# Optimization experiments

Measured on AMD Instinct MI355X. Metric: run time of the kernel, lower is better.

The kernel has to match this reference:

```python
import jax, jax.numpy as jnp
import numpy as np
import math

D_MODEL = 512
N_HEAD = 8
D_FF = 2048
B, S, S_ENC = 2, 2048, 2048
EPS = 1e-5


def _linear_params(key, d_in, d_out):
    kw, kb = jax.random.split(key)
    w = jax.random.normal(kw, (d_in, d_out), dtype=jnp.float32) * 0.02
    b = jax.random.normal(kb, (d_out,), dtype=jnp.float32) * 0.02
    return w, b


def setup_inputs() -> dict:
    key = jax.random.key(0)
    ks = jax.random.split(key, 16)
    dec = jax.random.normal(ks[0], (B, S, D_MODEL), dtype=jnp.float32)
    enc = jax.random.normal(ks[1], (B, S_ENC, D_MODEL), dtype=jnp.float32)
    src_mask = jnp.ones((B, 1, 1, S_ENC), dtype=jnp.int32)  # no padding
    tgt_mask = jnp.tril(jnp.ones((S, S), dtype=jnp.int32))[None, None]  # causal
    inp = {"dec": dec, "enc": enc, "src_mask": src_mask, "tgt_mask": tgt_mask}
    # self-attention projections
    for i, nm in enumerate(["sa_wq", "sa_wk", "sa_wv", "sa_wo"]):
        w, b = _linear_params(ks[2 + i], D_MODEL, D_MODEL)
        inp[nm], inp[nm.replace("w", "b")] = w, b
    # cross-attention projections
    for i, nm in enumerate(["ca_wq", "ca_wk", "ca_wv", "ca_wo"]):
        w, b = _linear_params(ks[6 + i], D_MODEL, D_MODEL)
        inp[nm], inp[nm.replace("w", "b")] = w, b
    # FFN
    inp["ffn_w1"], inp["ffn_b1"] = _linear_params(ks[10], D_MODEL, D_FF)
    inp["ffn_w2"], inp["ffn_b2"] = _linear_params(ks[11], D_FF, D_MODEL)
    # LayerNorms (gamma=1, beta=0 init as in torch)
    for i in (1, 2, 3):
        inp[f"ln{i}_g"] = jnp.ones((D_MODEL,), dtype=jnp.float32)
        inp[f"ln{i}_b"] = jnp.zeros((D_MODEL,), dtype=jnp.float32)
    return inp


def _layer_norm(x, g, b):
    mu = jnp.mean(x, axis=-1, keepdims=True)
    var = jnp.mean(jnp.square(x - mu), axis=-1, keepdims=True)
    return (x - mu) * jax.lax.rsqrt(var + EPS) * g + b


def _mha(xq, xkv, wq, bq, wk, bk, wv, bv, wo, bo, mask):
    Bq, Sq, D = xq.shape
    Sk = xkv.shape[1]
    d_k = D // N_HEAD
    def split(x, s):
        return x.reshape(x.shape[0], s, N_HEAD, d_k).transpose(0, 2, 1, 3)  # [B,H,S,dk]
    q = split(xq @ wq + bq, Sq)
    k = split(xkv @ wk + bk, Sk)
    v = split(xkv @ wv + bv, Sk)
    scores = jnp.einsum("bhqd,bhkd->bhqk", q, k) / math.sqrt(d_k)
    if mask is not None:
        scores = jnp.where(mask == 0, jnp.float32(-1e9), scores)
    attn = jax.nn.softmax(scores, axis=-1)
    out = jnp.einsum("bhqk,bhkd->bhqd", attn, v)
    out = out.transpose(0, 2, 1, 3).reshape(Bq, Sq, D)
    return out @ wo + bo


def reference(dec, enc, src_mask, tgt_mask,
              sa_wq, sa_bq, sa_wk, sa_bk, sa_wv, sa_bv, sa_wo, sa_bo,
              ca_wq, ca_bq, ca_wk, ca_bk, ca_wv, ca_bv, ca_wo, ca_bo,
              ffn_w1, ffn_b1, ffn_w2, ffn_b2,
              ln1_g, ln1_b, ln2_g, ln2_b, ln3_g, ln3_b):
    # dropout is identity in eval mode
    x = _mha(dec, dec, sa_wq, sa_bq, sa_wk, sa_bk, sa_wv, sa_bv, sa_wo, sa_bo, tgt_mask)
    x = _layer_norm(x + dec, ln1_g, ln1_b)
    _x = x
    x = _mha(x, enc, ca_wq, ca_bq, ca_wk, ca_bk, ca_wv, ca_bv, ca_wo, ca_bo, src_mask)
    x = _layer_norm(x + _x, ln2_g, ln2_b)
    _x = x
    x = jax.nn.relu(x @ ffn_w1 + ffn_b1) @ ffn_w2 + ffn_b2
    x = _layer_norm(x + _x, ln3_g, ln3_b)
    return x
```

## Files before the change

kernel.cpp:

```cpp
#include <hip/hip_runtime.h>


#define D_MODEL 512
#define NHEAD 8
#define DK 64
#define SEQ 2048
#define MTOK 4096
#define DFF 2048

typedef __attribute__((ext_vector_type(8))) short bf16x8;
typedef __attribute__((ext_vector_type(4))) float f32x4;

#if __has_builtin(__builtin_amdgcn_exp2f)
#define EXP2(x) __builtin_amdgcn_exp2f(x)
#else
#define EXP2(x) exp2f(x)
#endif

__device__ __forceinline__ unsigned short f2bf(float x) {
  unsigned u = __float_as_uint(x);
  u += 0x7FFF + ((u >> 16) & 1);
  return (unsigned short)(u >> 16);
}
__device__ __forceinline__ unsigned pack2(float a, float b) {
  return (unsigned)f2bf(a) | ((unsigned)f2bf(b) << 16);
}
__device__ __forceinline__ unsigned cvtpk(float lo, float hi) {
  unsigned r;
  asm("v_cvt_pk_bf16_f32 %0, %1, %2" : "=v"(r) : "v"(lo), "v"(hi));
  return r;
}
__device__ __forceinline__ void load_lds16(const unsigned short* g, unsigned short* l) {
  __builtin_amdgcn_global_load_lds(
      (const __attribute__((address_space(1))) void*)g,
      (__attribute__((address_space(3))) void*)l, 16, 0, 0);
}

struct WDesc { const float* src; unsigned short* dst; int K; int N; };
struct WPack { WDesc d[10]; };

__global__ __launch_bounds__(256)
void wprep_kernel(WPack p) {
  const WDesc wd = p.d[blockIdx.y];
  const int ntx = wd.N >> 5;
  const int ntile = (wd.K >> 5) * ntx;
  if ((int)blockIdx.x >= ntile) return;
  const int n0 = (blockIdx.x % ntx) * 32;
  const int k0 = (blockIdx.x / ntx) * 32;
  __shared__ float T[32][33];
  const int tid = threadIdx.x;
  {
    const int r = tid >> 3, c4 = (tid & 7) * 4;
    float4 v = *(const float4*)(wd.src + (long)(k0 + r) * wd.N + n0 + c4);
    T[r][c4] = v.x; T[r][c4 + 1] = v.y; T[r][c4 + 2] = v.z; T[r][c4 + 3] = v.w;
  }
  __syncthreads();
  {
    const int n = tid >> 3, kq = (tid & 7) * 4;
    ushort4 o;
    o.x = f2bf(T[kq + 0][n]); o.y = f2bf(T[kq + 1][n]);
    o.z = f2bf(T[kq + 2][n]); o.w = f2bf(T[kq + 3][n]);
    *(ushort4*)(wd.dst + (long)(n0 + n) * wd.K + k0 + kq) = o;
  }
}

__global__ __launch_bounds__(256)
void cast_kernel(const float* __restrict__ s, unsigned short* __restrict__ d, int n8) {
  const int i = blockIdx.x * 256 + threadIdx.x;
  if (i >= n8) return;
  float4 a = *(const float4*)(s + (long)i * 8);
  float4 b = *(const float4*)(s + (long)i * 8 + 4);
  uint4 o;
  o.x = pack2(a.x, a.y); o.y = pack2(a.z, a.w);
  o.z = pack2(b.x, b.y); o.w = pack2(b.z, b.w);
  *(uint4*)(d + (long)i * 8) = o;
}

template<int MODE, int BM, int BN>
__global__ __launch_bounds__(256)
void gemm_bf16(const unsigned short* __restrict__ A, const unsigned short* __restrict__ Wt,
               const float* __restrict__ b0, const float* __restrict__ b1,
               const float* __restrict__ b2, const float* res,
               const float* __restrict__ lnm, const float* __restrict__ lnr,
               const float* __restrict__ lng, const float* __restrict__ lnbt,
               unsigned short* __restrict__ o0, unsigned short* __restrict__ o1,
               unsigned short* __restrict__ o2, float* of,
               int M, int N, int K, float scale0) {
  constexpr int MF = BM / 32, NF = BN / 32;
  constexpr int AI = BM / 64, BI = BN / 64;
  __shared__ unsigned short As[BM * 32];
  __shared__ unsigned short Bs[BN * 32];
  const int tid = threadIdx.x;
  const int w = tid >> 6, lane = tid & 63, g = lane >> 4, li = lane & 15;
  const int m0 = blockIdx.x * BM, n0 = blockIdx.y * BN;
  const int wm = w >> 1, wn = w & 1;

  f32x4 acc[MF][NF] = {};
  const unsigned short* Ap[AI];
  const unsigned short* Bp[BI];
#pragma unroll
  for (int i = 0; i < AI; i++) {
    const int idx = i * 256 + tid;
    Ap[i] = A + (long)(m0 + (idx % BM)) * K + (idx / BM) * 8;
  }
#pragma unroll
  for (int i = 0; i < BI; i++) {
    const int idx = i * 256 + tid;
    Bp[i] = Wt + (long)(n0 + (idx % BN)) * K + (idx / BN) * 8;
  }

  for (int k0 = 0; k0 < K; k0 += 32) {
    __syncthreads();
#pragma unroll
    for (int i = 0; i < AI; i++) load_lds16(Ap[i] + k0, &As[(i * 256 + w * 64) * 8]);
#pragma unroll
    for (int i = 0; i < BI; i++) load_lds16(Bp[i] + k0, &Bs[(i * 256 + w * 64) * 8]);
    __syncthreads();
    bf16x8 af[MF], bfr[NF];
#pragma unroll
    for (int mf = 0; mf < MF; mf++)
      af[mf] = *(const bf16x8*)&As[(g * BM + wm * (BM / 2) + mf * 16 + li) * 8];
#pragma unroll
    for (int nf = 0; nf < NF; nf++)
      bfr[nf] = *(const bf16x8*)&Bs[(g * BN + wn * (BN / 2) + nf * 16 + li) * 8];
#pragma unroll
    for (int mf = 0; mf < MF; mf++)
#pragma unroll
      for (int nf = 0; nf < NF; nf++)
        acc[mf][nf] = __builtin_amdgcn_mfma_f32_16x16x32_bf16(af[mf], bfr[nf], acc[mf][nf], 0, 0, 0);
  }

#pragma unroll
  for (int nf = 0; nf < NF; nf++) {
    const int c = n0 + wn * (BN / 2) + nf * 16 + li;
    float bias, scl = 1.f;
    unsigned short* hdst = nullptr;
    float lngv = 0.f, lnbv = 0.f;
    if constexpr (MODE == 0) {
      const int which = c >> 9;
      bias = (which == 0 ? b0 : (which == 1 ? b1 : b2))[c & 511];
      if (which == 0) scl = scale0;
      hdst = which == 0 ? o0 : (which == 1 ? o1 : o2);
    } else {
      bias = b0[c];
      if constexpr (MODE == 3) { lngv = lng[c]; lnbv = lnbt[c]; }
    }
#pragma unroll
    for (int mf = 0; mf < MF; mf++) {
#pragma unroll
      for (int j = 0; j < 4; j++) {
        const int r = m0 + wm * (BM / 2) + mf * 16 + g * 4 + j;
        float v = acc[mf][nf][j] + bias;
        if constexpr (MODE == 0) {
          v *= scl;
          const int b = r >> 11, s = r & (SEQ - 1), h = (c >> 6) & 7, d = c & 63;
          hdst[(((long)(b * NHEAD + h)) * SEQ + s) * DK + d] = f2bf(v);
        } else if constexpr (MODE == 1) {
          v += res[(long)r * N + c];
          of[(long)r * N + c] = v;
        } else if constexpr (MODE == 2) {
          o0[(long)r * N + c] = f2bf(fmaxf(v, 0.f));
        } else {
          const float xr = res[(long)r * N + c];
          v += (xr - lnm[r]) * lnr[r] * lngv + lnbv;
          of[(long)r * N + c] = v;
        }
      }
    }
  }
}

template<bool CAUSAL>
__global__ __launch_bounds__(256)
void attn_bf16(const unsigned short* __restrict__ Qg, const unsigned short* __restrict__ Kg,
               const unsigned short* __restrict__ Vg, float* __restrict__ Opart,
               float* __restrict__ Mst, float* __restrict__ Lst) {
  __shared__ unsigned short SM[16384];
  unsigned short* const Qp = SM;
  unsigned short* const Kp = SM + 8192;
  unsigned short* const Vt = SM + 12288;
  const int tid = threadIdx.x;
  const int w = tid >> 6, lane = tid & 63, g = lane >> 4, li = lane & 15;
  const int qb = blockIdx.x, bh = blockIdx.y, ck = blockIdx.z;
  const int q0 = qb * 128;
  const long base = (long)bh * SEQ * DK;
  unsigned short* const Pl = SM + w * 2048;

#pragma unroll
  for (int i = 0; i < 4; i++) {
    const int idx = i * 256 + tid;
    const int dg = idx >> 7, q = idx & 127;
    load_lds16(Qg + base + (long)(q0 + q) * DK + dg * 8, &Qp[(i * 256 + w * 64) * 8]);
  }
  __syncthreads();
  bf16x8 bq[2][2];
#pragma unroll
  for (int qf = 0; qf < 2; qf++)
#pragma unroll
    for (int ks = 0; ks < 2; ks++)
      bq[qf][ks] = *(const bf16x8*)&Qp[((ks * 4 + g) * 128 + w * 32 + qf * 16 + li) * 8];

  f32x4 oacc[2][4] = {};
  float mrun[2] = {-1e30f, -1e30f};
  float denom[2] = {0.f, 0.f};

  const int vdg = tid >> 5;
  const int vs0 = (tid & 31) * 2;
  const int vsg = vs0 >> 3, vso = vs0 & 7;

  const int tbeg = CAUSAL ? ck : ck * 8;
  const int tend = CAUSAL ? (2 * qb + 2) : (ck * 8 + 8);
  const int tstep = CAUSAL ? 4 : 1;
  for (int t = tbeg; t < tend; t += tstep) {
    const int k0 = t * 64;
    __syncthreads();
#pragma unroll
    for (int i = 0; i < 2; i++) {
      const int idx = i * 256 + tid;
      const int dg = idx >> 6, kk = idx & 63;
      load_lds16(Kg + base + (long)(k0 + kk) * DK + dg * 8, &Kp[(i * 256 + w * 64) * 8]);
    }
    {
      const unsigned short* vsrc = Vg + base + (long)(k0 + vs0) * DK + vdg * 8;
      uint4 r0 = *(const uint4*)vsrc;
      uint4 r1 = *(const uint4*)(vsrc + DK);
      unsigned short u0[8], u1[8];
      *(uint4*)u0 = r0; *(uint4*)u1 = r1;
#pragma unroll
      for (int e = 0; e < 8; e++) {
        const int d = vdg * 8 + e;
        const int dsw = d ^ (vsg & 7);
        *(unsigned*)&Vt[(vsg * 64 + dsw) * 8 + vso] =
            (unsigned)u0[e] | ((unsigned)u1[e] << 16);
      }
    }
    __syncthreads();

    f32x4 sacc[4][2] = {};
#pragma unroll
    for (int ks = 0; ks < 2; ks++) {
#pragma unroll
      for (int kf = 0; kf < 4; kf++) {
        bf16x8 ka = *(const bf16x8*)&Kp[((ks * 4 + g) * 64 + kf * 16 + li) * 8];
#pragma unroll
        for (int qf = 0; qf < 2; qf++)
          sacc[kf][qf] = __builtin_amdgcn_mfma_f32_16x16x32_bf16(ka, bq[qf][ks], sacc[kf][qf], 0, 0, 0);
      }
    }
    if (CAUSAL && t >= 2 * qb) {
#pragma unroll
      for (int kf = 0; kf < 4; kf++)
#pragma unroll
        for (int qf = 0; qf < 2; qf++)
#pragma unroll
          for (int j = 0; j < 4; j++) {
            const int kg_ = k0 + kf * 16 + g * 4 + j;
            const int qg_ = q0 + w * 32 + qf * 16 + li;
            if (kg_ > qg_) sacc[kf][qf][j] = -1e30f;
          }
    }
    float mx[2];
#pragma unroll
    for (int qf = 0; qf < 2; qf++) {
      float a = fmaxf(fmaxf(sacc[0][qf][0], sacc[0][qf][1]), fmaxf(sacc[0][qf][2], sacc[0][qf][3]));
      float b = fmaxf(fmaxf(sacc[1][qf][0], sacc[1][qf][1]), fmaxf(sacc[1][qf][2], sacc[1][qf][3]));
      float c = fmaxf(fmaxf(sacc[2][qf][0], sacc[2][qf][1]), fmaxf(sacc[2][qf][2], sacc[2][qf][3]));
      float d = fmaxf(fmaxf(sacc[3][qf][0], sacc[3][qf][1]), fmaxf(sacc[3][qf][2], sacc[3][qf][3]));
      float m_ = fmaxf(fmaxf(a, b), fmaxf(c, d));
      m_ = fmaxf(m_, __shfl_xor(m_, 16, 64));
      m_ = fmaxf(m_, __shfl_xor(m_, 32, 64));
      mx[qf] = m_;
    }
    const int full = !__all((mx[0] - mrun[0] <= 8.f) && (mx[1] - mrun[1] <= 8.f));
    float corrv[2] = {1.f, 1.f};
    if (full) {
#pragma unroll
      for (int qf = 0; qf < 2; qf++) {
        const float mn = fmaxf(mrun[qf], mx[qf]);
        corrv[qf] = EXP2(mrun[qf] - mn);
        mrun[qf] = mn;
      }
    }
#pragma unroll
    for (int qf = 0; qf < 2; qf++) {
      float ps = 0.f;
#pragma unroll
      for (int kf = 0; kf < 4; kf++)
#pragma unroll
        for (int j = 0; j < 4; j++) {
          const float p = EXP2(sacc[kf][qf][j] - mrun[qf]);
          sacc[kf][qf][j] = p;
          ps += p;
        }
      ps += __shfl_xor(ps, 16, 64);
      ps += __shfl_xor(ps, 32, 64);
      denom[qf] = denom[qf] * corrv[qf] + ps;
    }
    if (full) {
#pragma unroll
      for (int mf = 0; mf < 2; mf++)
#pragma unroll
        for (int j = 0; j < 4; j++) {
          const float cf = __shfl(corrv[mf], g * 4 + j, 64);
#pragma unroll
          for (int df = 0; df < 4; df++) oacc[mf][df][j] *= cf;
        }
    }
#pragma unroll
    for (int kf = 0; kf < 4; kf++)
#pragma unroll
      for (int qf = 0; qf < 2; qf++) {
        uint2 pv;
        pv.x = cvtpk(sacc[kf][qf][0], sacc[kf][qf][1]);
        pv.y = cvtpk(sacc[kf][qf][2], sacc[kf][qf][3]);
        *(uint2*)&Pl[((kf * 2 + (g >> 1)) * 32 + qf * 16 + li) * 8 + (g & 1) * 4] = pv;
      }
#pragma unroll
    for (int ks2 = 0; ks2 < 2; ks2++) {
      const int sg = ks2 * 4 + g;
#pragma unroll
      for (int mf = 0; mf < 2; mf++) {
        bf16x8 pa = *(const bf16x8*)&Pl[(sg * 32 + mf * 16 + li) * 8];
#pragma unroll
        for (int df = 0; df < 4; df++) {
          bf16x8 vb = *(const bf16x8*)&Vt[(sg * 64 + ((df * 16 + li) ^ (sg & 7))) * 8];
          oacc[mf][df] = __builtin_amdgcn_mfma_f32_16x16x32_bf16(pa, vb, oacc[mf][df], 0, 0, 0);
        }
      }
    }
  }

  const long pbase = (long)(ck * 16 + bh) * SEQ;
  if (g == 0) {
#pragma unroll
    for (int qf = 0; qf < 2; qf++) {
      const int q = q0 + w * 32 + qf * 16 + li;
      Mst[pbase + q] = mrun[qf];
      Lst[pbase + q] = denom[qf];
    }
  }
#pragma unroll
  for (int mf = 0; mf < 2; mf++)
#pragma unroll
    for (int j = 0; j < 4; j++) {
      const int q = q0 + w * 32 + mf * 16 + g * 4 + j;
      float* op = Opart + (pbase + q) * 64;
#pragma unroll
      for (int df = 0; df < 4; df++) op[df * 16 + li] = oacc[mf][df][j];
    }
}

__global__ __launch_bounds__(256)
void combine_kernel(const float* __restrict__ Opart, const float* __restrict__ Mst,
                    const float* __restrict__ Lst, unsigned short* __restrict__ AOb) {
  const int row = blockIdx.x * 4 + (threadIdx.x >> 6);
  const int lane = threadIdx.x & 63;
  const int bh = row >> 11, q = row & (SEQ - 1);
  float m[4], l[4], mstar = -1e30f;
#pragma unroll
  for (int c = 0; c < 4; c++) {
    m[c] = Mst[((long)c * 16 + bh) * SEQ + q];
    l[c] = Lst[((long)c * 16 + bh) * SEQ + q];
    mstar = fmaxf(mstar, m[c]);
  }
  float den = 0.f, o = 0.f;
#pragma unroll
  for (int c = 0; c < 4; c++) {
    const float wgt = EXP2(m[c] - mstar);
    den += wgt * l[c];
    o += wgt * Opart[(((long)c * 16 + bh) * SEQ + q) * 64 + lane];
  }
  const int b = bh >> 3, h = bh & 7;
  AOb[((long)(b * SEQ + q)) * D_MODEL + h * DK + lane] = f2bf(o / den);
}

template<int V>
__global__ __launch_bounds__(256)
void ln_kernel(const float* __restrict__ x, const float* __restrict__ gam,
               const float* __restrict__ bet, float* __restrict__ outf,
               unsigned short* __restrict__ outb, float* __restrict__ mu_s,
               float* __restrict__ rs_s) {
  const int row = blockIdx.x * 4 + (threadIdx.x >> 6);
  const int lane = threadIdx.x & 63;
  const float* xr = x + (long)row * D_MODEL;
  float4 v0 = *(const float4*)&xr[lane * 8];
  float4 v1 = *(const float4*)&xr[lane * 8 + 4];
  float xv[8] = {v0.x, v0.y, v0.z, v0.w, v1.x, v1.y, v1.z, v1.w};
  float s = 0.f, s2 = 0.f;
#pragma unroll
  for (int i = 0; i < 8; i++) { s += xv[i]; s2 = fmaf(xv[i], xv[i], s2); }
#pragma unroll
  for (int off = 32; off > 0; off >>= 1) {
    s += __shfl_xor(s, off, 64);
    s2 += __shfl_xor(s2, off, 64);
  }
  const float mu = s * (1.f / D_MODEL);
  const float var = fmaxf(s2 * (1.f / D_MODEL) - mu * mu, 0.f);
  const float rstd = rsqrtf(var + 1e-5f);
  float y[8];
#pragma unroll
  for (int i = 0; i < 8; i++) {
    const int c = lane * 8 + i;
    y[i] = (xv[i] - mu) * rstd * gam[c] + bet[c];
  }
  if constexpr (V == 0) {
    uint4 o;
    o.x = pack2(y[0], y[1]); o.y = pack2(y[2], y[3]);
    o.z = pack2(y[4], y[5]); o.w = pack2(y[6], y[7]);
    *(uint4*)(outb + (long)row * D_MODEL + lane * 8) = o;
    if (lane == 0) { mu_s[row] = mu; rs_s[row] = rstd; }
  } else {
    float* orow = outf + (long)row * D_MODEL + lane * 8;
    *(float4*)orow = make_float4(y[0], y[1], y[2], y[3]);
    *(float4*)(orow + 4) = make_float4(y[4], y[5], y[6], y[7]);
  }
}

extern "C" void kernel_launch(void* const* d_in, const int* in_sizes, int n_in,
                              void* d_out, int out_size, void* d_ws, size_t ws_size,
                              hipStream_t stream) {
  const float* dec = (const float*)d_in[0];
  const float* enc = (const float*)d_in[1];
  const float* sa_wq = (const float*)d_in[4];
  const float* sa_bq = (const float*)d_in[5];
  const float* sa_wk = (const float*)d_in[6];
  const float* sa_bk = (const float*)d_in[7];
  const float* sa_wv = (const float*)d_in[8];
  const float* sa_bv = (const float*)d_in[9];
  const float* sa_wo = (const float*)d_in[10];
  const float* sa_bo = (const float*)d_in[11];
  const float* ca_wq = (const float*)d_in[12];
  const float* ca_bq = (const float*)d_in[13];
  const float* ca_wk = (const float*)d_in[14];
  const float* ca_bk = (const float*)d_in[15];
  const float* ca_wv = (const float*)d_in[16];
  const float* ca_bv = (const float*)d_in[17];
  const float* ca_wo = (const float*)d_in[18];
  const float* ca_bo = (const float*)d_in[19];
  const float* ffn_w1 = (const float*)d_in[20];
  const float* ffn_b1 = (const float*)d_in[21];
  const float* ffn_w2 = (const float*)d_in[22];
  const float* ffn_b2 = (const float*)d_in[23];
  const float* ln1_g = (const float*)d_in[24];
  const float* ln1_b = (const float*)d_in[25];
  const float* ln2_g = (const float*)d_in[26];
  const float* ln2_b = (const float*)d_in[27];
  const float* ln3_g = (const float*)d_in[28];
  const float* ln3_b = (const float*)d_in[29];

  char* wsb = (char*)d_ws;
  unsigned short* dec_bf = (unsigned short*)wsb;
  float* Opart = (float*)wsb;
  float* Mst = (float*)(wsb + 33554432);
  float* Lst = (float*)(wsb + 34078720);
  unsigned short* MIDb = (unsigned short*)wsb;
  size_t off = 34603008;
  unsigned short* qkv_t = (unsigned short*)(wsb + off); off += 1572864;
  unsigned short* wo_t  = (unsigned short*)(wsb + off); off += 524288;
  unsigned short* cq_t  = (unsigned short*)(wsb + off); off += 524288;
  unsigned short* ckv_t = (unsigned short*)(wsb + off); off += 1048576;
  unsigned short* co_t  = (unsigned short*)(wsb + off); off += 524288;
  unsigned short* f1_t  = (unsigned short*)(wsb + off); off += 2097152;
  unsigned short* f2_t  = (unsigned short*)(wsb + off); off += 2097152;
  unsigned short* enc_bf = (unsigned short*)(wsb + off); off += 4194304;
  unsigned short* Qb  = (unsigned short*)(wsb + off); off += 4194304;
  unsigned short* Kb  = (unsigned short*)(wsb + off); off += 4194304;
  unsigned short* Vb  = (unsigned short*)(wsb + off); off += 4194304;
  unsigned short* AOb = (unsigned short*)(wsb + off); off += 4194304;
  unsigned short* X1b = (unsigned short*)(wsb + off); off += 4194304;
  unsigned short* X2b = (unsigned short*)(wsb + off); off += 4194304;
  float* R   = (float*)(wsb + off); off += 8388608;
  float* mu1 = (float*)(wsb + off); off += 16384;
  float* rs1 = (float*)(wsb + off); off += 16384;
  float* mu2 = (float*)(wsb + off); off += 16384;
  float* rs2 = (float*)(wsb + off); off += 16384;

  dim3 blk(256);
  const float QS = 0.125f * 1.44269504f;

  WPack wp;
  wp.d[0] = {sa_wq, qkv_t, 512, 512};
  wp.d[1] = {sa_wk, qkv_t + 262144, 512, 512};
  wp.d[2] = {sa_wv, qkv_t + 524288, 512, 512};
  wp.d[3] = {sa_wo, wo_t, 512, 512};
  wp.d[4] = {ca_wq, cq_t, 512, 512};
  wp.d[5] = {ca_wk, ckv_t, 512, 512};
  wp.d[6] = {ca_wv, ckv_t + 262144, 512, 512};
  wp.d[7] = {ca_wo, co_t, 512, 512};
  wp.d[8] = {ffn_w1, f1_t, 512, 2048};
  wp.d[9] = {ffn_w2, f2_t, 2048, 512};
  wprep_kernel<<<dim3(1024, 10), blk, 0, stream>>>(wp);
  cast_kernel<<<1024, blk, 0, stream>>>(dec, dec_bf, 262144);
  cast_kernel<<<1024, blk, 0, stream>>>(enc, enc_bf, 262144);

  gemm_bf16<0, 128, 128><<<dim3(32, 12), blk, 0, stream>>>(dec_bf, qkv_t, sa_bq, sa_bk, sa_bv,
      nullptr, nullptr, nullptr, nullptr, nullptr, Qb, Kb, Vb, nullptr, MTOK, 1536, 512, QS);
  attn_bf16<true><<<dim3(16, 16, 4), blk, 0, stream>>>(Qb, Kb, Vb, Opart, Mst, Lst);
  combine_kernel<<<8192, blk, 0, stream>>>(Opart, Mst, Lst, AOb);
  gemm_bf16<1, 128, 64><<<dim3(32, 8), blk, 0, stream>>>(AOb, wo_t, sa_bo, nullptr, nullptr,
      dec, nullptr, nullptr, nullptr, nullptr, nullptr, nullptr, nullptr, R, MTOK, 512, 512, 1.f);
  ln_kernel<0><<<1024, blk, 0, stream>>>(R, ln1_g, ln1_b, nullptr, X1b, mu1, rs1);

  gemm_bf16<0, 128, 64><<<dim3(32, 8), blk, 0, stream>>>(X1b, cq_t, ca_bq, nullptr, nullptr,
      nullptr, nullptr, nullptr, nullptr, nullptr, Qb, nullptr, nullptr, nullptr, MTOK, 512, 512, QS);
  gemm_bf16<0, 128, 128><<<dim3(32, 8), blk, 0, stream>>>(enc_bf, ckv_t, ca_bk, ca_bv, nullptr,
      nullptr, nullptr, nullptr, nullptr, nullptr, Kb, Vb, nullptr, nullptr, MTOK, 1024, 512, 1.f);
  attn_bf16<false><<<dim3(16, 16, 4), blk, 0, stream>>>(Qb, Kb, Vb, Opart, Mst, Lst);
  combine_kernel<<<8192, blk, 0, stream>>>(Opart, Mst, Lst, AOb);
  gemm_bf16<3, 128, 64><<<dim3(32, 8), blk, 0, stream>>>(AOb, co_t, ca_bo, nullptr, nullptr,
      R, mu1, rs1, ln1_g, ln1_b, nullptr, nullptr, nullptr, R, MTOK, 512, 512, 1.f);
  ln_kernel<0><<<1024, blk, 0, stream>>>(R, ln2_g, ln2_b, nullptr, X2b, mu2, rs2);

  gemm_bf16<2, 128, 128><<<dim3(32, 16), blk, 0, stream>>>(X2b, f1_t, ffn_b1, nullptr, nullptr,
      nullptr, nullptr, nullptr, nullptr, nullptr, MIDb, nullptr, nullptr, nullptr, MTOK, 2048, 512, 1.f);
  gemm_bf16<3, 128, 64><<<dim3(32, 8), blk, 0, stream>>>(MIDb, f2_t, ffn_b2, nullptr, nullptr,
      R, mu2, rs2, ln2_g, ln2_b, nullptr, nullptr, nullptr, R, MTOK, 512, 2048, 1.f);
  ln_kernel<1><<<1024, blk, 0, stream>>>(R, ln3_g, ln3_b, (float*)d_out, nullptr, nullptr, nullptr);
}
```

Baseline: 435.5 us.

## Double-buffer LDS tiles with K-step 64 in bf16 GEMM

```diff
diff --git a/kernel.cpp b/kernel.cpp
--- a/kernel.cpp
+++ b/kernel.cpp
@@ -87,9 +87,12 @@
                unsigned short* __restrict__ o2, float* of,
                int M, int N, int K, float scale0) {
   constexpr int MF = BM / 32, NF = BN / 32;
-  constexpr int AI = BM / 64, BI = BN / 64;
-  __shared__ unsigned short As[BM * 32];
-  __shared__ unsigned short Bs[BN * 32];
+  constexpr int AI = BM / 32;
+  constexpr int BI = BN / 32;
+  __shared__ unsigned short As0[BM * 64];
+  __shared__ unsigned short As1[BM * 64];
+  __shared__ unsigned short Bs0[BN * 64];
+  __shared__ unsigned short Bs1[BN * 64];
   const int tid = threadIdx.x;
   const int w = tid >> 6, lane = tid & 63, g = lane >> 4, li = lane & 15;
   const int m0 = blockIdx.x * BM, n0 = blockIdx.y * BN;
@@ -108,27 +111,44 @@
     const int idx = i * 256 + tid;
     Bp[i] = Wt + (long)(n0 + (idx % BN)) * K + (idx / BN) * 8;
   }
-
-  for (int k0 = 0; k0 < K; k0 += 32) {
+  const int nt = K >> 6;
+
+#define G_STAGE(t, Ad, Bd)                                               \
+  {                                                                      \
+    _Pragma("unroll") for (int i = 0; i < AI; i++)                       \
+        load_lds16(Ap[i] + (t) * 64, &Ad[(i * 256 + w * 64) * 8]);       \
+    _Pragma("unroll") for (int i = 0; i < BI; i++)                       \
+        load_lds16(Bp[i] + (t) * 64, &Bd[(i * 256 + w * 64) * 8]);       \
+  }
+
+#define G_COMP(Ad, Bd)                                                            \
+  {                                                                               \
+    _Pragma("unroll") for (int s = 0; s < 2; s++) {                               \
+      bf16x8 af[MF], bfr[NF];                                                     \
+      _Pragma("unroll") for (int mf = 0; mf < MF; mf++)                           \
+          af[mf] = *(const bf16x8*)&Ad[((s * 4 + g) * BM + wm * (BM / 2) + mf * 16 + li) * 8]; \
+      _Pragma("unroll") for (int nf = 0; nf < NF; nf++)                           \
+          bfr[nf] = *(const bf16x8*)&Bd[((s * 4 + g) * BN + wn * (BN / 2) + nf * 16 + li) * 8]; \
+      _Pragma("unroll") for (int mf = 0; mf < MF; mf++)                           \
+          _Pragma("unroll") for (int nf = 0; nf < NF; nf++)                       \
+              acc[mf][nf] = __builtin_amdgcn_mfma_f32_16x16x32_bf16(af[mf], bfr[nf], acc[mf][nf], 0, 0, 0); \
+    }                                                                             \
+  }
+
+  G_STAGE(0, As0, Bs0);
+  __syncthreads();
+  for (int t = 0; t < nt; t += 2) {
+    if (t + 1 < nt) G_STAGE(t + 1, As1, Bs1);
+    G_COMP(As0, Bs0);
     __syncthreads();
-#pragma unroll
-    for (int i = 0; i < AI; i++) load_lds16(Ap[i] + k0, &As[(i * 256 + w * 64) * 8]);
-#pragma unroll
-    for (int i = 0; i < BI; i++) load_lds16(Bp[i] + k0, &Bs[(i * 256 + w * 64) * 8]);
-    __syncthreads();
-    bf16x8 af[MF], bfr[NF];
-#pragma unroll
-    for (int mf = 0; mf < MF; mf++)
-      af[mf] = *(const bf16x8*)&As[(g * BM + wm * (BM / 2) + mf * 16 + li) * 8];
-#pragma unroll
-    for (int nf = 0; nf < NF; nf++)
-      bfr[nf] = *(const bf16x8*)&Bs[(g * BN + wn * (BN / 2) + nf * 16 + li) * 8];
-#pragma unroll
-    for (int mf = 0; mf < MF; mf++)
-#pragma unroll
-      for (int nf = 0; nf < NF; nf++)
-        acc[mf][nf] = __builtin_amdgcn_mfma_f32_16x16x32_bf16(af[mf], bfr[nf], acc[mf][nf], 0, 0, 0);
-  }
+    if (t + 1 < nt) {
+      if (t + 2 < nt) G_STAGE(t + 2, As0, Bs0);
+      G_COMP(As1, Bs1);
+      __syncthreads();
+    }
+  }
+#undef G_STAGE
+#undef G_COMP
 
 #pragma unroll
   for (int nf = 0; nf < NF; nf++) {
```

Result: faster. 409.2 us (-6.0%).
